# Kernel tuning notes

Measured on AMD Instinct MI355X. Metric: run time of the kernel, lower is better.

The kernel has to match this reference:

```python
import jax, jax.numpy as jnp
import numpy as np

K = 20
EPS = 1e-5
NEG_SLOPE = 0.2


def get_graph_feature(x, k):
    # x: (B, C, N). Build kNN graph from negative squared distances.
    xx = jnp.sum(x * x, axis=1)                       # (B, N)
    inner = jnp.einsum('bcn,bcm->bnm', x, x)          # (B, N, N)
    neg_dist = 2.0 * inner - xx[:, :, None] - xx[:, None, :]
    idx = jax.lax.top_k(neg_dist, k)[1]               # (B, N, k) int32
    # gather neighbor features: (B, C, N, k)
    feat = jnp.take_along_axis(x[:, :, None, :], idx[:, None, :, :], axis=3)
    center = x[:, :, :, None]
    return jnp.concatenate([feat - center, jnp.broadcast_to(center, feat.shape)], axis=1)


def conv_bn_lrelu(e, W, b, gamma, beta, mean, var):
    # e: (B, 2C, N, k); W: (O, 2C) 1x1 conv kernel
    y = jnp.einsum('oc,bcnk->bonk', W, e) + b[None, :, None, None]
    inv = gamma / jnp.sqrt(var + EPS)
    y = y * inv[None, :, None, None] + (beta - mean * inv)[None, :, None, None]
    y = jnp.where(y > 0, y, NEG_SLOPE * y)
    return jnp.max(y, axis=-1)                         # (B, O, N)


def setup_inputs() -> dict:
    key = jax.random.key(0)
    ks = jax.random.split(key, 32)
    B, C0, N = 8, 3, 4096
    dims_in = [2 * C0, 2 * 64, 2 * 64]
    dims_out = [64, 64, 128]
    inp = {"x": jax.random.normal(ks[0], (B, C0, N), dtype=jnp.float32)}
    ki = 1
    for i, (ci, co) in enumerate(zip(dims_in, dims_out)):
        inp[f"W{i}"] = jax.random.normal(ks[ki], (co, ci), dtype=jnp.float32) * (1.0 / np.sqrt(ci)); ki += 1
        inp[f"b{i}"] = jax.random.normal(ks[ki], (co,), dtype=jnp.float32) * 0.01; ki += 1
        inp[f"gamma{i}"] = jnp.ones((co,), dtype=jnp.float32)
        inp[f"beta{i}"] = jnp.zeros((co,), dtype=jnp.float32)
        inp[f"mean{i}"] = jax.random.normal(ks[ki], (co,), dtype=jnp.float32) * 0.01; ki += 1
        inp[f"var{i}"] = jax.random.uniform(ks[ki], (co,), dtype=jnp.float32) + 0.5; ki += 1
    return inp


def reference(x, W0, b0, gamma0, beta0, mean0, var0,
              W1, b1, gamma1, beta1, mean1, var1,
              W2, b2, gamma2, beta2, mean2, var2):
    layers = [(W0, b0, gamma0, beta0, mean0, var0),
              (W1, b1, gamma1, beta1, mean1, var1),
              (W2, b2, gamma2, beta2, mean2, var2)]
    for (W, b, g, be, m, v) in layers:
        e = get_graph_feature(x, K)
        x = conv_bn_lrelu(e, W, b, g, be, m, v)
    return x
```

## Files before the change

### kernel.cpp

```cpp
#include <hip/hip_runtime.h>


#define NPTS 4096
#define NB 8
#define KK 20

__device__ __forceinline__ void topk_insert(float v, int gi, float (&tv)[KK], int (&ti)[KK]) {
#pragma unroll
    for (int j = KK - 1; j >= 1; --j) {
        if (v > tv[j - 1])      { tv[j] = tv[j - 1]; ti[j] = ti[j - 1]; }
        else if (v > tv[j])     { tv[j] = v;         ti[j] = gi; }
    }
    if (v > tv[0]) { tv[0] = v; ti[0] = gi; }
}

template <int C, int CO>
__global__ __launch_bounds__(256) void prep_kernel(
    const float* __restrict__ x, const float* __restrict__ W,
    const float* __restrict__ bias, const float* __restrict__ gam,
    const float* __restrict__ bet, const float* __restrict__ mean,
    const float* __restrict__ var,
    float* __restrict__ Z, float* __restrict__ T)
{
    constexpr int OS = CO / 16;
    __shared__ float xs[C][64];
    __shared__ float w1s[C][CO];
    __shared__ float wds[C][CO];
    const int tid = threadIdx.x;
    const int b  = blockIdx.y;
    const int n0 = blockIdx.x * 64;

    for (int i = tid; i < C * 64; i += 256)
        xs[i >> 6][i & 63] = x[((size_t)b * C + (i >> 6)) * NPTS + n0 + (i & 63)];
    for (int i = tid; i < C * CO; i += 256) {
        const int c = i / CO, o = i - c * CO;
        const float w1 = W[o * (2 * C) + c];
        const float w2 = W[o * (2 * C) + C + c];
        w1s[c][o] = w1;
        wds[c][o] = w2 - w1;
    }
    __syncthreads();

    const int to = tid & 15, tn = tid >> 4;
    float az[4][OS], at[4][OS];
#pragma unroll
    for (int i = 0; i < 4; ++i)
#pragma unroll
        for (int j = 0; j < OS; ++j) { az[i][j] = 0.f; at[i][j] = 0.f; }

#pragma unroll 4
    for (int c = 0; c < C; ++c) {
        float xv[4];
#pragma unroll
        for (int i = 0; i < 4; ++i) xv[i] = xs[c][tn * 4 + i];
#pragma unroll
        for (int j = 0; j < OS; ++j) {
            const float a1 = w1s[c][j * 16 + to];
            const float ad = wds[c][j * 16 + to];
#pragma unroll
            for (int i = 0; i < 4; ++i) { az[i][j] += a1 * xv[i]; at[i][j] += ad * xv[i]; }
        }
    }

#pragma unroll
    for (int j = 0; j < OS; ++j) {
        const int o = j * 16 + to;
        const float inv = gam[o] / sqrtf(var[o] + 1e-5f);
        const float sh  = bet[o] - mean[o] * inv;
        const float bo  = bias[o];
#pragma unroll
        for (int i = 0; i < 4; ++i) {
            const int n = n0 + tn * 4 + i;
            const size_t base = ((size_t)b * NPTS + n) * CO + o;
            Z[base] = az[i][j] * inv;
            T[base] = (at[i][j] + bo) * inv + sh;
        }
    }
}

template <int C>
__global__ __launch_bounds__(512) void knn_kernel(
    const float* __restrict__ x, int* __restrict__ nbr)
{
    constexpr int DP = 132;
    constexpr int MAIN  = 2 * C * 128 + 128 * DP;
    constexpr int MERGE = 2 * 128 * 85;
    constexpr int SW = (MAIN > MERGE) ? MAIN : MERGE;
    constexpr int NPF = (C * 128 + 2047) / 2048;
    __shared__ __align__(16) float smem[SW];
    float* rowX = smem;
    float* colX = smem + C * 128;
    float* dist = smem + 2 * C * 128;

    const int tid = threadIdx.x;
    const int b  = blockIdx.y;
    const int n0 = blockIdx.x * 128;
    const int tc = tid & 31, tr = tid >> 5;
    const int prow = tid >> 2, pslot = tid & 3;
    const float* xb = x + (size_t)b * C * NPTS;

    float tkv[KK]; int tki[KK];
#pragma unroll
    for (int j = 0; j < KK; ++j) { tkv[j] = -3.0e38f; tki[j] = 0; }

    for (int i = tid * 4; i < C * 128; i += 2048)
        *(float4*)&rowX[i] = *(const float4*)&xb[(size_t)(i >> 7) * NPTS + n0 + (i & 127)];

    float4 pf[NPF];
#pragma unroll
    for (int u = 0; u < NPF; ++u) {
        const int i = tid * 4 + u * 2048;
        if (i < C * 128) pf[u] = *(const float4*)&xb[(size_t)(i >> 7) * NPTS + (i & 127)];
    }

    for (int t = 0; t < NPTS / 128; ++t) {
        const int m0 = t * 128;
        const int m0n = (m0 + 128) & (NPTS - 1);
        __syncthreads();
#pragma unroll
        for (int u = 0; u < NPF; ++u) {
            const int i = tid * 4 + u * 2048;
            if (i < C * 128) *(float4*)&colX[i] = pf[u];
        }
#pragma unroll
        for (int u = 0; u < NPF; ++u) {
            const int i = tid * 4 + u * 2048;
            if (i < C * 128) pf[u] = *(const float4*)&xb[(size_t)(i >> 7) * NPTS + m0n + (i & 127)];
        }
        __syncthreads();

        float acc[8][4];
#pragma unroll
        for (int i = 0; i < 8; ++i)
#pragma unroll
            for (int j = 0; j < 4; ++j) acc[i][j] = 0.f;

#pragma unroll 4
        for (int c = 0; c < C; ++c) {
            const float4 a0 = *(const float4*)&rowX[c * 128 + tr * 8];
            const float4 a1 = *(const float4*)&rowX[c * 128 + tr * 8 + 4];
            const float4 b4 = *(const float4*)&colX[c * 128 + tc * 4];
            const float av[8] = {a0.x, a0.y, a0.z, a0.w, a1.x, a1.y, a1.z, a1.w};
            const float bv[4] = {b4.x, b4.y, b4.z, b4.w};
#pragma unroll
            for (int i = 0; i < 8; ++i)
#pragma unroll
                for (int j = 0; j < 4; ++j) {
                    const float d = av[i] - bv[j];
                    acc[i][j] += d * d;
                }
        }
#pragma unroll
        for (int i = 0; i < 8; ++i) {
            const int r = tr * 8 + i;
            float4 w;
            w.x = -acc[i][0];
            w.y = -acc[i][1];
            w.z = -acc[i][2];
            w.w = -acc[i][3];
            *(float4*)&dist[r * DP + tc * 4] = w;
        }
        __syncthreads();

        unsigned mask = 0u;
        const float thr = tkv[KK - 1];
        const float* drow = dist + prow * DP + pslot * 32;
        const int rot = (prow + 8 * pslot) & 31;
#pragma unroll
        for (int jj = 0; jj < 32; ++jj) {
            const int cc = (jj + rot) & 31;
            mask |= ((unsigned)(drow[cc] > thr)) << cc;
        }
        const int gb = m0 + pslot * 32;
        while (mask) {
            const int cc = __ffs(mask) - 1;
            mask &= mask - 1;
            const float v = drow[cc];
            if (v > tkv[KK - 1]) topk_insert(v, gb + cc, tkv, tki);
        }
    }
    __syncthreads();

    float* mv = smem;
    int*   mi = (int*)(smem + 128 * 85);
    const int mbase = prow * 85 + pslot * 21;
#pragma unroll
    for (int j = 0; j < KK; ++j) { mv[mbase + j] = tkv[j]; mi[mbase + j] = tki[j]; }
    mv[mbase + KK] = -3.0e38f;
    mi[mbase + KK] = 0x7fffffff;
    __syncthreads();
    if (tid < 128) {
        int* orow = nbr + ((size_t)b * NPTS + n0 + tid) * KK;
        const int rb = tid * 85;
        int p0 = rb, p1 = rb + 21, p2 = rb + 42, p3 = rb + 63;
        float v0 = mv[p0], v1 = mv[p1], v2 = mv[p2], v3 = mv[p3];
        int   i0 = mi[p0], i1 = mi[p1], i2 = mi[p2], i3 = mi[p3];
#pragma unroll 1
        for (int k = 0; k < KK; ++k) {
            float best = v0; int bi = i0; int bs = 0;
            if (v1 > best || (v1 == best && i1 < bi)) { best = v1; bi = i1; bs = 1; }
            if (v2 > best || (v2 == best && i2 < bi)) { best = v2; bi = i2; bs = 2; }
            if (v3 > best || (v3 == best && i3 < bi)) { best = v3; bi = i3; bs = 3; }
            orow[k] = bi;
            if (bs == 0)      { ++p0; v0 = mv[p0]; i0 = mi[p0]; }
            else if (bs == 1) { ++p1; v1 = mv[p1]; i1 = mi[p1]; }
            else if (bs == 2) { ++p2; v2 = mv[p2]; i2 = mi[p2]; }
            else              { ++p3; v3 = mv[p3]; i3 = mi[p3]; }
        }
    }
}

template <int CO>
__global__ __launch_bounds__(256) void gather_kernel(
    const float* __restrict__ Z, const float* __restrict__ T,
    const int* __restrict__ nbr, float* __restrict__ out)
{
    constexpr int CQ = CO / 4;
    __shared__ int idxl[64 * 21];
    const int tid = threadIdx.x;
    const int b  = blockIdx.y;
    const int n0 = blockIdx.x * 64;

    for (int i = tid; i < 64 * KK; i += 256) {
        const int n = i / KK, k2 = i - n * KK;
        idxl[n * 21 + k2] = nbr[((size_t)b * NPTS + n0) * KK + i];
    }
    __syncthreads();

    const int og = tid >> 6;
    const int ns = tid & 63;
    const float* Tb = T + ((size_t)b * NPTS + n0 + ns) * CO + og * CQ;
    float tv[CQ];
#pragma unroll
    for (int j = 0; j < CQ; j += 4) {
        const float4 q = *(const float4*)&Tb[j];
        tv[j] = q.x; tv[j + 1] = q.y; tv[j + 2] = q.z; tv[j + 3] = q.w;
    }
    float acc[CQ];
#pragma unroll
    for (int j = 0; j < CQ; ++j) acc[j] = -3.0e38f;

    const float* Zb = Z + (size_t)b * NPTS * CO + og * CQ;
#pragma unroll 1
    for (int k2 = 0; k2 < KK; ++k2) {
        const int m = idxl[ns * 21 + k2];
        const float* zr = Zb + (size_t)m * CO;
#pragma unroll
        for (int j = 0; j < CQ; j += 4) {
            const float4 z4 = *(const float4*)&zr[j];
            float v;
            v = z4.x + tv[j];     v = v > 0.f ? v : 0.2f * v; acc[j]     = fmaxf(acc[j], v);
            v = z4.y + tv[j + 1]; v = v > 0.f ? v : 0.2f * v; acc[j + 1] = fmaxf(acc[j + 1], v);
            v = z4.z + tv[j + 2]; v = v > 0.f ? v : 0.2f * v; acc[j + 2] = fmaxf(acc[j + 2], v);
            v = z4.w + tv[j + 3]; v = v > 0.f ? v : 0.2f * v; acc[j + 3] = fmaxf(acc[j + 3], v);
        }
    }
#pragma unroll
    for (int j = 0; j < CQ; ++j)
        out[((size_t)b * CO + og * CQ + j) * NPTS + n0 + ns] = acc[j];
}

extern "C" void kernel_launch(void* const* d_in, const int* in_sizes, int n_in,
                              void* d_out, int out_size, void* d_ws, size_t ws_size,
                              hipStream_t stream)
{
    const float* x0  = (const float*)d_in[0];
    const float* W0  = (const float*)d_in[1];
    const float* b0  = (const float*)d_in[2];
    const float* g0  = (const float*)d_in[3];
    const float* be0 = (const float*)d_in[4];
    const float* mn0 = (const float*)d_in[5];
    const float* vr0 = (const float*)d_in[6];
    const float* W1  = (const float*)d_in[7];
    const float* b1  = (const float*)d_in[8];
    const float* g1  = (const float*)d_in[9];
    const float* be1 = (const float*)d_in[10];
    const float* mn1 = (const float*)d_in[11];
    const float* vr1 = (const float*)d_in[12];
    const float* W2  = (const float*)d_in[13];
    const float* b2  = (const float*)d_in[14];
    const float* g2  = (const float*)d_in[15];
    const float* be2 = (const float*)d_in[16];
    const float* mn2 = (const float*)d_in[17];
    const float* vr2 = (const float*)d_in[18];

    float* ws = (float*)d_ws;
    float* Z  = ws;
    float* Tt = Z  + (size_t)NB * NPTS * 128;
    int*   nb = (int*)(Tt + (size_t)NB * NPTS * 128);
    float* xA = (float*)(nb + (size_t)NB * NPTS * KK);
    float* xB = xA;
    float* op = (float*)d_out;
    (void)in_sizes; (void)n_in; (void)out_size; (void)ws_size;

    const dim3 blk(256), blkK(512);
    const dim3 gP(64, NB), gKn(32, NB), gG(64, NB);

    prep_kernel<3, 64><<<gP, blk, 0, stream>>>(x0, W0, b0, g0, be0, mn0, vr0, Z, Tt);
    knn_kernel<3><<<gKn, blkK, 0, stream>>>(x0, nb);
    gather_kernel<64><<<gG, blk, 0, stream>>>(Z, Tt, nb, xA);

    prep_kernel<64, 64><<<gP, blk, 0, stream>>>(xA, W1, b1, g1, be1, mn1, vr1, Z, Tt);
    knn_kernel<64><<<gKn, blkK, 0, stream>>>(xA, nb);
    gather_kernel<64><<<gG, blk, 0, stream>>>(Z, Tt, nb, xB);

    prep_kernel<64, 128><<<gP, blk, 0, stream>>>(xB, W2, b2, g2, be2, mn2, vr2, Z, Tt);
    knn_kernel<64><<<gKn, blkK, 0, stream>>>(xB, nb);
    gather_kernel<128><<<gG, blk, 0, stream>>>(Z, Tt, nb, op);
}
```

Before: 1.695 ms.

## Split kNN distance channel reduction across two thread halves with 8x8 tiles

The kNN distance tile is now computed with 8x8 register tiles per thread. The channel dimension is split between two halves of the 512-thread block, and each half computes a partial sum over its channel range. The first half writes its partial sums to shared memory, and after a barrier the second half adds its own and writes the negated distance. This raises arithmetic per shared-memory load and halves the serial channel loop per thread. The cost is an extra barrier, a shared-memory read-modify-write pass, and higher register use per thread.

```diff
diff --git a/kernel.cpp b/kernel.cpp
--- a/kernel.cpp
+++ b/kernel.cpp
@@ -87,6 +87,7 @@
     constexpr int MERGE = 2 * 128 * 85;
     constexpr int SW = (MAIN > MERGE) ? MAIN : MERGE;
     constexpr int NPF = (C * 128 + 2047) / 2048;
+    constexpr int CH = (C + 1) / 2;
     __shared__ __align__(16) float smem[SW];
     float* rowX = smem;
     float* colX = smem + C * 128;
@@ -95,7 +96,10 @@
     const int tid = threadIdx.x;
     const int b  = blockIdx.y;
     const int n0 = blockIdx.x * 128;
-    const int tc = tid & 31, tr = tid >> 5;
+    const int cs  = tid >> 8;
+    const int t2  = tid & 255;
+    const int tr8 = t2 >> 4;
+    const int tc8 = t2 & 15;
     const int prow = tid >> 2, pslot = tid & 3;
     const float* xb = x + (size_t)b * C * NPTS;
 
@@ -112,6 +116,11 @@
         const int i = tid * 4 + u * 2048;
         if (i < C * 128) pf[u] = *(const float4*)&xb[(size_t)(i >> 7) * NPTS + (i & 127)];
     }
+
+    const int c0   = cs ? CH : 0;
+    const int trip = cs ? (C - CH) : CH;
+    const float* rA = rowX + (size_t)c0 * 128 + tr8 * 8;
+    const float* cB = colX + (size_t)c0 * 128 + tc8 * 4;
 
     for (int t = 0; t < NPTS / 128; ++t) {
         const int m0 = t * 128;
@@ -129,36 +138,54 @@
         }
         __syncthreads();
 
-        float acc[8][4];
+        float acc[8][8];
 #pragma unroll
         for (int i = 0; i < 8; ++i)
 #pragma unroll
-            for (int j = 0; j < 4; ++j) acc[i][j] = 0.f;
-
-#pragma unroll 4
-        for (int c = 0; c < C; ++c) {
-            const float4 a0 = *(const float4*)&rowX[c * 128 + tr * 8];
-            const float4 a1 = *(const float4*)&rowX[c * 128 + tr * 8 + 4];
-            const float4 b4 = *(const float4*)&colX[c * 128 + tc * 4];
+            for (int j = 0; j < 8; ++j) acc[i][j] = 0.f;
+
+#pragma unroll 2
+        for (int k = 0; k < trip; ++k) {
+            const float4 a0 = *(const float4*)&rA[k * 128];
+            const float4 a1 = *(const float4*)&rA[k * 128 + 4];
+            const float4 b0 = *(const float4*)&cB[k * 128];
+            const float4 b1 = *(const float4*)&cB[k * 128 + 64];
             const float av[8] = {a0.x, a0.y, a0.z, a0.w, a1.x, a1.y, a1.z, a1.w};
-            const float bv[4] = {b4.x, b4.y, b4.z, b4.w};
+            const float bv[8] = {b0.x, b0.y, b0.z, b0.w, b1.x, b1.y, b1.z, b1.w};
 #pragma unroll
             for (int i = 0; i < 8; ++i)
 #pragma unroll
-                for (int j = 0; j < 4; ++j) {
+                for (int j = 0; j < 8; ++j) {
                     const float d = av[i] - bv[j];
                     acc[i][j] += d * d;
                 }
         }
-#pragma unroll
-        for (int i = 0; i < 8; ++i) {
-            const int r = tr * 8 + i;
-            float4 w;
-            w.x = -acc[i][0];
-            w.y = -acc[i][1];
-            w.z = -acc[i][2];
-            w.w = -acc[i][3];
-            *(float4*)&dist[r * DP + tc * 4] = w;
+
+        if (cs == 0) {
+#pragma unroll
+            for (int i = 0; i < 8; ++i) {
+                const int r = tr8 * 8 + i;
+                float4 w0, w1;
+                w0.x = acc[i][0]; w0.y = acc[i][1]; w0.z = acc[i][2]; w0.w = acc[i][3];
+                w1.x = acc[i][4]; w1.y = acc[i][5]; w1.z = acc[i][6]; w1.w = acc[i][7];
+                *(float4*)&dist[r * DP + tc8 * 4]      = w0;
+                *(float4*)&dist[r * DP + 64 + tc8 * 4] = w1;
+            }
+        }
+        __syncthreads();
+        if (cs == 1) {
+#pragma unroll
+            for (int i = 0; i < 8; ++i) {
+                const int r = tr8 * 8 + i;
+                float4 p0 = *(const float4*)&dist[r * DP + tc8 * 4];
+                float4 p1 = *(const float4*)&dist[r * DP + 64 + tc8 * 4];
+                p0.x = -(p0.x + acc[i][0]); p0.y = -(p0.y + acc[i][1]);
+                p0.z = -(p0.z + acc[i][2]); p0.w = -(p0.w + acc[i][3]);
+                p1.x = -(p1.x + acc[i][4]); p1.y = -(p1.y + acc[i][5]);
+                p1.z = -(p1.z + acc[i][6]); p1.w = -(p1.w + acc[i][7]);
+                *(float4*)&dist[r * DP + tc8 * 4]      = p0;
+                *(float4*)&dist[r * DP + 64 + tc8 * 4] = p1;
+            }
         }
         __syncthreads();
 
```

New measurement: 1.723 ms. About the same (+1.6%).
